# Optimization experiments

Hardware: AMD Instinct MI355X
Metric: run time of the kernel (lower is better)

Reference implementation:

```python
import jax, jax.numpy as jnp
import numpy as np

B, C, H, W = 8, 256, 64, 64
CK = C // 8  # query/key channels


def setup_inputs() -> dict:
    key = jax.random.key(0)
    ks = jax.random.split(key, 8)
    s = 1.0 / np.sqrt(C)
    return {
        "x": jax.random.normal(ks[0], (B, C, H, W), dtype=jnp.float32),
        "Wq": jax.random.normal(ks[1], (CK, C), dtype=jnp.float32) * s,
        "bq": jax.random.normal(ks[2], (CK,), dtype=jnp.float32) * 0.01,
        "Wk": jax.random.normal(ks[3], (CK, C), dtype=jnp.float32) * s,
        "bk": jax.random.normal(ks[4], (CK,), dtype=jnp.float32) * 0.01,
        "Wv": jax.random.normal(ks[5], (C, C), dtype=jnp.float32) * s,
        "bv": jax.random.normal(ks[6], (C,), dtype=jnp.float32) * 0.01,
        "gamma": jax.random.normal(ks[7], (1,), dtype=jnp.float32) * 0.1,
    }


def reference(x, Wq, bq, Wk, bk, Wv, bv, gamma):
    b, c, h, w = x.shape
    n = h * w
    xf = x.reshape(b, c, n)                       # [B,C,N]
    # 1x1 convs == channel-wise linear maps
    q = jnp.einsum('oc,bcn->bon', Wq, xf) + bq[:, None]   # [B,CK,N]
    k = jnp.einsum('oc,bcn->bon', Wk, xf) + bk[:, None]   # [B,CK,N]
    v = jnp.einsum('oc,bcn->bon', Wv, xf) + bv[:, None]   # [B,C,N]
    energy = jnp.einsum('bcm,bcn->bmn', q, k)             # [B,N,N] (query rows m)
    attn = jax.nn.softmax(energy, axis=-1)
    out = jnp.einsum('bcn,bmn->bcm', v, attn)             # value @ attn^T
    out = out.reshape(b, c, h, w)
    return gamma * out + x
```

## Files before the change

### kernel.cpp

```cpp
#include <hip/hip_runtime.h>
#include <stdint.h>

typedef unsigned short u16;
typedef unsigned int u32;
typedef __bf16 bf16_t;
typedef __bf16 bf16x4 __attribute__((ext_vector_type(4)));
typedef __bf16 bf16x8 __attribute__((ext_vector_type(8)));
typedef float f32x4 __attribute__((ext_vector_type(4)));
typedef float f32x16 __attribute__((ext_vector_type(16)));

#define LOG2E 1.4426950408889634f
#define MFMA32(a, b, c) __builtin_amdgcn_mfma_f32_32x32x16_bf16(a, b, c, 0, 0, 0)

__device__ __forceinline__ u16 f2bf(float f) {
    union { float f; unsigned int u; } v; v.f = f;
    unsigned int r = v.u + 0x7fffu + ((v.u >> 16) & 1u);
    return (u16)(r >> 16);
}

__device__ __forceinline__ bf16x8 ld8f_bf(const float* __restrict__ p) {
    float4 a = *reinterpret_cast<const float4*>(p);
    float4 b = *reinterpret_cast<const float4*>(p + 4);
    bf16x8 r;
    r[0] = (bf16_t)a.x; r[1] = (bf16_t)a.y; r[2] = (bf16_t)a.z; r[3] = (bf16_t)a.w;
    r[4] = (bf16_t)b.x; r[5] = (bf16_t)b.y; r[6] = (bf16_t)b.z; r[7] = (bf16_t)b.w;
    return r;
}

__device__ __forceinline__ u32 cvt_pk_bf16(float a, float b) {
    u32 r;
    asm("v_cvt_pk_bf16_f32 %0, %1, %2" : "=v"(r) : "v"(a), "v"(b));
    return r;
}

__device__ __forceinline__ void plane32_swap(u32& a, u32& b) {
    asm("v_permlane32_swap_b32 %0, %1" : "+v"(a), "+v"(b));
}

__device__ __forceinline__ bf16x8 pack8(const float* p) {
    u32 c0 = cvt_pk_bf16(p[0], p[1]);
    u32 c1 = cvt_pk_bf16(p[2], p[3]);
    u32 c2 = cvt_pk_bf16(p[4], p[5]);
    u32 c3 = cvt_pk_bf16(p[6], p[7]);
    plane32_swap(c0, c2);
    plane32_swap(c1, c3);
    union { u32 u[4]; bf16x8 v; } f;
    f.u[0] = c0; f.u[1] = c1; f.u[2] = c2; f.u[3] = c3;
    return f.v;
}

__device__ __forceinline__ void g2lds16(const u16* g, u16* l) {
    __builtin_amdgcn_global_load_lds(
        (const __attribute__((address_space(1))) unsigned int*)g,
        (__attribute__((address_space(3))) unsigned int*)l, 16, 0, 0);
}

__global__ __launch_bounds__(256) void k_transpose(
    const float* __restrict__ x,
    const float* __restrict__ Wq, const float* __restrict__ Wk,
    const float* __restrict__ Wv,
    u16* __restrict__ xT, u16* __restrict__ wqkb, u16* __restrict__ wvb) {
    int blk = blockIdx.x;
    int t = threadIdx.x;
    if (blk >= 2048) {
        if (blk == 2048) {
            for (int j = 0; j < 8; ++j) {
                int fg = j * 256 + t;
                int n = fg >> 5, g = fg & 31;
                const float* src = (n < 32) ? (Wq + (size_t)n * 256 + g * 8)
                                            : (Wk + (size_t)(n - 32) * 256 + g * 8);
                *reinterpret_cast<bf16x8*>(wqkb + n * 256 + ((g ^ (n & 7)) << 3)) =
                    ld8f_bf(src);
            }
        } else {
            int base = (blk - 2049) * 2048;
            for (int j = 0; j < 8; ++j) {
                int fg = base + j * 256 + t;
                int slice = fg >> 10, d = fg & 1023;
                int co = d >> 2, g2 = (d & 3) ^ (co & 3);
                *reinterpret_cast<bf16x8*>(wvb + fg * 8) =
                    ld8f_bf(Wv + (size_t)co * 256 + slice * 32 + g2 * 8);
            }
        }
        return;
    }
    __shared__ u16 tile[64][68];
    int b = blk >> 8;
    int r = blk & 255;
    int c0 = (r & 3) * 64;
    int n0 = (r >> 2) * 64;
    const float* xb = x + (size_t)b * 256 * 4096;
    u16* xTb = xT + (size_t)b * 4096 * 256;
    int lc = t >> 4;
    int l4 = (t & 15) * 4;
    #pragma unroll
    for (int p = 0; p < 4; ++p) {
        int c = lc + p * 16;
        float4 v = *reinterpret_cast<const float4*>(xb + (size_t)(c0 + c) * 4096 + n0 + l4);
        tile[c][l4 + 0] = f2bf(v.x); tile[c][l4 + 1] = f2bf(v.y);
        tile[c][l4 + 2] = f2bf(v.z); tile[c][l4 + 3] = f2bf(v.w);
    }
    __syncthreads();
    #pragma unroll
    for (int p = 0; p < 4; ++p) {
        int n = lc + p * 16;
        ushort4 v;
        v.x = tile[l4 + 0][n]; v.y = tile[l4 + 1][n];
        v.z = tile[l4 + 2][n]; v.w = tile[l4 + 3][n];
        int gslot = ((c0 + l4) >> 3) ^ ((n0 + n) & 7);
        *reinterpret_cast<ushort4*>(
            xTb + (size_t)(n0 + n) * 256 + (gslot << 3) + (l4 & 7)) = v;
    }
}

__global__ __launch_bounds__(256, 2) void k_proj(
    const u16* __restrict__ xT, const u16* __restrict__ wqkb,
    const u16* __restrict__ wvb,
    const float* __restrict__ bq, const float* __restrict__ bk,
    const float* __restrict__ bv,
    u16* __restrict__ qt, u16* __restrict__ kt, u16* __restrict__ vt) {
    __shared__ u16 Xs[64 * 256];
    __shared__ u16 Ws[64 * 256];
    __shared__ u16 Wvs[256 * 32];
    int blk = blockIdx.x;
    int b = blk & 7;
    int n0 = (blk >> 3) * 64;
    int t = threadIdx.x;
    int w = t >> 6;
    int lane = t & 63;
    int lo = lane & 15;
    int q = lane >> 4;
    const u16* xTb = xT + (size_t)b * 4096 * 256;

    #pragma unroll
    for (int p = 0; p < 8; ++p) {
        g2lds16(xTb + (size_t)n0 * 256 + (p * 256 + t) * 8, &Xs[(p * 256 + w * 64) * 8]);
        g2lds16(wqkb + (p * 256 + t) * 8, &Ws[(p * 256 + w * 64) * 8]);
    }

    f32x4 accqk[4] = {};
    f32x4 accv[16];
    #pragma unroll
    for (int i = 0; i < 16; ++i) accv[i] = f32x4{0.f, 0.f, 0.f, 0.f};

    int rowA = w * 16 + lo;
    int cw = w * 64;
    for (int c0 = 0; c0 < 256; c0 += 32) {
        __syncthreads();
        #pragma unroll
        for (int p = 0; p < 4; ++p) {
            g2lds16(wvb + (size_t)(c0 >> 5) * 8192 + (p * 256 + t) * 8,
                    &Wvs[(p * 256 + w * 64) * 8]);
        }
        __syncthreads();

        int K = c0 >> 3;
        bf16x8 a = *reinterpret_cast<const bf16x8*>(
            &Xs[(rowA * 32 + ((K + q) ^ (lo & 7))) * 8]);
        #pragma unroll
        for (int ot = 0; ot < 4; ++ot) {
            bf16x8 bb = *reinterpret_cast<const bf16x8*>(
                &Ws[((ot * 16 + lo) * 32 + ((K + q) ^ (lo & 7))) * 8]);
            accqk[ot] = __builtin_amdgcn_mfma_f32_16x16x32_bf16(a, bb, accqk[ot], 0, 0, 0);
        }
        bf16x8 xbf[4];
        #pragma unroll
        for (int nt = 0; nt < 4; ++nt)
            xbf[nt] = *reinterpret_cast<const bf16x8*>(
                &Xs[((nt * 16 + lo) * 32 + ((K + q) ^ (lo & 7))) * 8]);
        #pragma unroll
        for (int ct = 0; ct < 4; ++ct) {
            int co = cw + ct * 16 + lo;
            bf16x8 av = *reinterpret_cast<const bf16x8*>(
                &Wvs[(co * 4 + (q ^ (co & 3))) * 8]);
            #pragma unroll
            for (int nt = 0; nt < 4; ++nt)
                accv[ct * 4 + nt] = __builtin_amdgcn_mfma_f32_16x16x32_bf16(
                    av, xbf[nt], accv[ct * 4 + nt], 0, 0, 0);
        }
    }
    #pragma unroll
    for (int ot = 0; ot < 4; ++ot) {
        float bias = (ot < 2) ? bq[ot * 16 + lo] : bk[(ot - 2) * 16 + lo];
        #pragma unroll
        for (int r = 0; r < 4; ++r) {
            int n = n0 + w * 16 + q * 4 + r;
            float val = accqk[ot][r] + bias;
            if (ot < 2) qt[((size_t)b * 4096 + n) * 32 + ot * 16 + lo] = f2bf(val * LOG2E);
            else        kt[((size_t)b * 4096 + n) * 32 + (ot - 2) * 16 + lo] = f2bf(val);
        }
    }
    #pragma unroll
    for (int ct = 0; ct < 4; ++ct) {
        #pragma unroll
        for (int nt = 0; nt < 4; ++nt) {
            int nt_g = (n0 >> 4) + nt;
            #pragma unroll
            for (int r = 0; r < 4; ++r) {
                int co = cw + ct * 16 + q * 4 + r;
                float val = accv[ct * 4 + nt][r] + bv[co];
                vt[(((size_t)b * 256 + nt_g) * 256 + co) * 16 + lo] = f2bf(val);
            }
        }
    }
}

#define FLASH_PV_HALF1(FC0, FC1, Vc_)                                          \
    {                                                                          \
        bf16x8 v0_ = *reinterpret_cast<const bf16x8*>(Vc_ + gslot8);           \
        bf16x8 v1_ = *reinterpret_cast<const bf16x8*>(Vc_ + 512 + gslot8);     \
        bf16x8 v2_ = *reinterpret_cast<const bf16x8*>(Vc_ + 1024 + gslot8);    \
        bf16x8 v3_ = *reinterpret_cast<const bf16x8*>(Vc_ + 1536 + gslot8);    \
        O0 = MFMA32(v0_, FC0, O0); O1 = MFMA32(v1_, FC0, O1);                  \
        O2 = MFMA32(v2_, FC0, O2); O3 = MFMA32(v3_, FC0, O3);                  \
        bf16x8 v4_ = *reinterpret_cast<const bf16x8*>(Vc_ + 2048 + gslot8);    \
        bf16x8 v5_ = *reinterpret_cast<const bf16x8*>(Vc_ + 2560 + gslot8);    \
        bf16x8 v6_ = *reinterpret_cast<const bf16x8*>(Vc_ + 3072 + gslot8);    \
        bf16x8 v7_ = *reinterpret_cast<const bf16x8*>(Vc_ + 3584 + gslot8);    \
        O0 = MFMA32(v4_, FC1, O0); O1 = MFMA32(v5_, FC1, O1);                  \
        O2 = MFMA32(v6_, FC1, O2); O3 = MFMA32(v7_, FC1, O3);                  \
    }

#define FLASH_PV_HALF2(FC2, FC3, Vc_)                                          \
    {                                                                          \
        bf16x8 v0_ = *reinterpret_cast<const bf16x8*>(Vc_ + 4096 + gslot8);    \
        bf16x8 v1_ = *reinterpret_cast<const bf16x8*>(Vc_ + 4608 + gslot8);    \
        bf16x8 v2_ = *reinterpret_cast<const bf16x8*>(Vc_ + 5120 + gslot8);    \
        bf16x8 v3_ = *reinterpret_cast<const bf16x8*>(Vc_ + 5632 + gslot8);    \
        O0 = MFMA32(v0_, FC2, O0); O1 = MFMA32(v1_, FC2, O1);                  \
        O2 = MFMA32(v2_, FC2, O2); O3 = MFMA32(v3_, FC2, O3);                  \
        bf16x8 v4_ = *reinterpret_cast<const bf16x8*>(Vc_ + 6144 + gslot8);    \
        bf16x8 v5_ = *reinterpret_cast<const bf16x8*>(Vc_ + 6656 + gslot8);    \
        bf16x8 v6_ = *reinterpret_cast<const bf16x8*>(Vc_ + 7168 + gslot8);    \
        bf16x8 v7_ = *reinterpret_cast<const bf16x8*>(Vc_ + 7680 + gslot8);    \
        O0 = MFMA32(v4_, FC3, O0); O1 = MFMA32(v5_, FC3, O1);                  \
        O2 = MFMA32(v6_, FC3, O2); O3 = MFMA32(v7_, FC3, O3);                  \
    }

#define FLASH_ITER(S_, KC0, KC1, KC2, KC3, KN0, KN1, KN2, KN3,                 \
                   FC0, FC1, FC2, FC3, FN0, FN1, FN2, FN3, VDN)                \
    {                                                                          \
        const int s_ = (S_);                                                   \
        const u16* kp_ = kbase + (size_t)(((s_ + 2) & 63) * 2048);             \
        KN0 = *reinterpret_cast<const bf16x8*>(kp_);                           \
        KN1 = *reinterpret_cast<const bf16x8*>(kp_ + 16);                      \
        KN2 = *reinterpret_cast<const bf16x8*>(kp_ + 1024);                    \
        KN3 = *reinterpret_cast<const bf16x8*>(kp_ + 1040);                    \
        const u16* vs_ = vstage + (size_t)(s_ + 1) * 16384;                    \
        g2lds16(vs_,        VDN);                                              \
        g2lds16(vs_ + 512,  VDN + 512);                                        \
        g2lds16(vs_ + 1024, VDN + 1024);                                       \
        g2lds16(vs_ + 1536, VDN + 1536);                                       \
        f32x16 S0_ = MFMA32(KC0, qf0, z16); S0_ = MFMA32(KC1, qf1, S0_);       \
        f32x16 S1_ = MFMA32(KC2, qf0, z16); S1_ = MFMA32(KC3, qf1, S1_);       \
        const u16* Vc_ = Vs[s_ & 1];                                           \
        float p0_[16];                                                         \
        _Pragma("unroll")                                                      \
        for (int i_ = 0; i_ < 16; ++i_) {                                      \
            p0_[i_] = __builtin_amdgcn_exp2f(S0_[i_]); lsum += p0_[i_];        \
        }                                                                      \
        FN0 = pack8(p0_); FN1 = pack8(p0_ + 8);                                \
        FLASH_PV_HALF1(FC0, FC1, Vc_)                                          \
        float p1_[16];                                                         \
        _Pragma("unroll")                                                      \
        for (int i_ = 0; i_ < 16; ++i_) {                                      \
            p1_[i_] = __builtin_amdgcn_exp2f(S1_[i_]); lsum += p1_[i_];        \
        }                                                                      \
        FN2 = pack8(p1_); FN3 = pack8(p1_ + 8);                                \
        FLASH_PV_HALF2(FC2, FC3, Vc_)                                          \
        __syncthreads();                                                       \
    }

__global__ __launch_bounds__(256, 2) void k_flash(
    const u16* __restrict__ qt, const u16* __restrict__ kt,
    const u16* __restrict__ vt, const float* __restrict__ x,
    const float* __restrict__ gamma, float* __restrict__ out) {
    __shared__ u16 Vs[2][8192];
    int blk = blockIdx.x;
    int b = blk & 7;
    int rest = blk >> 3;
    int m0 = (rest & 31) * 128;
    int ch0 = (rest >> 5) * 128;
    int t = threadIdx.x;
    int w = t >> 6;
    int lane = t & 63;
    int la = lane & 31;
    int hi = lane >> 5;

    const u16* qtb = qt + (size_t)b * 4096 * 32;
    const u16* ktb = kt + (size_t)b * 4096 * 32;
    const u16* vtb = vt + (size_t)b * 256 * 256 * 16;

    int qw0 = m0 + w * 32;
    bf16x8 qf0 = *reinterpret_cast<const bf16x8*>(qtb + (size_t)(qw0 + la) * 32 + hi * 8);
    bf16x8 qf1 = *reinterpret_cast<const bf16x8*>(qtb + (size_t)(qw0 + la) * 32 + 16 + hi * 8);

    const u16* kbase = ktb + (size_t)la * 32 + hi * 8;

    int g = la * 2 + hi;
    int gslot8 = (g ^ (g >> 3)) * 8;
    int sg = lane ^ (lane >> 3);
    const u16* vstage = vtb + ((size_t)(w * 256) + ch0) * 16 + sg * 8;
    u16* vd0 = &Vs[0][w * 2048];
    u16* vd1 = &Vs[1][w * 2048];

    f32x16 O0 = {}, O1 = {}, O2 = {}, O3 = {};
    const f32x16 z16 = {};
    float lsum = 0.f;

    bf16x8 kA0, kA1, kA2, kA3, kB0, kB1, kB2, kB3;
    bf16x8 fA0, fA1, fA2, fA3, fB0, fB1, fB2, fB3;

    kA0 = *reinterpret_cast<const bf16x8*>(kbase);
    kA1 = *reinterpret_cast<const bf16x8*>(kbase + 16);
    kA2 = *reinterpret_cast<const bf16x8*>(kbase + 1024);
    kA3 = *reinterpret_cast<const bf16x8*>(kbase + 1040);
    g2lds16(vstage,        vd0);
    g2lds16(vstage + 512,  vd0 + 512);
    g2lds16(vstage + 1024, vd0 + 1024);
    g2lds16(vstage + 1536, vd0 + 1536);
    kB0 = *reinterpret_cast<const bf16x8*>(kbase + 2048);
    kB1 = *reinterpret_cast<const bf16x8*>(kbase + 2064);
    kB2 = *reinterpret_cast<const bf16x8*>(kbase + 3072);
    kB3 = *reinterpret_cast<const bf16x8*>(kbase + 3088);
    {
        f32x16 S0 = MFMA32(kA0, qf0, z16); S0 = MFMA32(kA1, qf1, S0);
        f32x16 S1 = MFMA32(kA2, qf0, z16); S1 = MFMA32(kA3, qf1, S1);
        float p0[16], p1[16];
        #pragma unroll
        for (int i = 0; i < 16; ++i) { p0[i] = __builtin_amdgcn_exp2f(S0[i]); lsum += p0[i]; }
        fA0 = pack8(p0); fA1 = pack8(p0 + 8);
        #pragma unroll
        for (int i = 0; i < 16; ++i) { p1[i] = __builtin_amdgcn_exp2f(S1[i]); lsum += p1[i]; }
        fA2 = pack8(p1); fA3 = pack8(p1 + 8);
    }
    __syncthreads();

    for (int ss = 0; ss < 31; ++ss) {
        int s0 = ss * 2;
        FLASH_ITER(s0,     kB0, kB1, kB2, kB3, kA0, kA1, kA2, kA3,
                           fA0, fA1, fA2, fA3, fB0, fB1, fB2, fB3, vd1)
        FLASH_ITER(s0 + 1, kA0, kA1, kA2, kA3, kB0, kB1, kB2, kB3,
                           fB0, fB1, fB2, fB3, fA0, fA1, fA2, fA3, vd0)
    }
    FLASH_ITER(62, kB0, kB1, kB2, kB3, kA0, kA1, kA2, kA3,
                   fA0, fA1, fA2, fA3, fB0, fB1, fB2, fB3, vd1)
    {
        const u16* Vc_ = Vs[1];
        FLASH_PV_HALF1(fB0, fB1, Vc_)
        FLASH_PV_HALF2(fB2, fB3, Vc_)
    }

    lsum += __shfl_xor(lsum, 32, 64);
    float linv = 1.0f / lsum;
    float gm = gamma[0];
    const float* xb = x + (size_t)b * 256 * 4096;
    float* ob = out + (size_t)b * 256 * 4096;
    int m = m0 + w * 32 + la;
    #pragma unroll
    for (int r = 0; r < 16; ++r) {
        int crow = (r & 3) + 8 * (r >> 2) + 4 * hi;
        size_t i0 = (size_t)(ch0 + crow) * 4096 + m;
        ob[i0]             = gm * (O0[r] * linv) + xb[i0];
        ob[i0 + 32 * 4096] = gm * (O1[r] * linv) + xb[i0 + 32 * 4096];
        ob[i0 + 64 * 4096] = gm * (O2[r] * linv) + xb[i0 + 64 * 4096];
        ob[i0 + 96 * 4096] = gm * (O3[r] * linv) + xb[i0 + 96 * 4096];
    }
}

extern "C" void kernel_launch(void* const* d_in, const int* in_sizes, int n_in,
                              void* d_out, int out_size, void* d_ws, size_t ws_size,
                              hipStream_t stream) {
    const float* x     = (const float*)d_in[0];
    const float* Wq    = (const float*)d_in[1];
    const float* bq    = (const float*)d_in[2];
    const float* Wk    = (const float*)d_in[3];
    const float* bk    = (const float*)d_in[4];
    const float* Wv    = (const float*)d_in[5];
    const float* bv    = (const float*)d_in[6];
    const float* gamma = (const float*)d_in[7];
    float* out = (float*)d_out;

    char* ws = (char*)d_ws;
    u16* xT   = (u16*)d_out;
    u16* wqkb = (u16*)d_out + 8388608;
    u16* wvb  = (u16*)d_out + 8388608 + 16384;
    u16* qt = (u16*)ws;
    u16* kt = (u16*)(ws + 2097152);
    u16* vt = (u16*)(ws + 2 * 2097152);

    k_transpose<<<2053, 256, 0, stream>>>(x, Wq, Wk, Wv, xT, wqkb, wvb);
    k_proj<<<512, 256, 0, stream>>>(xT, wqkb, wvb, bq, bk, bv, qt, kt, vt);
    k_flash<<<512, 256, 0, stream>>>(qt, kt, vt, x, gamma, out);
}
```

Measured before the change: 199.9 us.

## Halve flash channel tile to double grid; widen proj block to 128 positions

The flash kernel now gives each block 64 output channels instead of 128. That doubles the grid to 1024 blocks, halves the V staging in LDS and the output accumulators, and raises the occupancy hint to 4. The aim is better latency hiding and more waves per CU, at the cost of recomputing QK^T and the exponentials twice as often per query tile. The projection kernel switches to 512 threads covering 128 positions per block, so the Wq/Wk and Wv weight tiles are reused across more positions. s_setprio is wrapped around the PV MFMA groups to favour matrix issue.

```diff
diff --git a/kernel.cpp b/kernel.cpp
--- a/kernel.cpp
+++ b/kernel.cpp
@@ -113,18 +113,18 @@
     }
 }
 
-__global__ __launch_bounds__(256, 2) void k_proj(
+__global__ __launch_bounds__(512, 2) void k_proj(
     const u16* __restrict__ xT, const u16* __restrict__ wqkb,
     const u16* __restrict__ wvb,
     const float* __restrict__ bq, const float* __restrict__ bk,
     const float* __restrict__ bv,
     u16* __restrict__ qt, u16* __restrict__ kt, u16* __restrict__ vt) {
-    __shared__ u16 Xs[64 * 256];
+    __shared__ u16 Xs[128 * 256];
     __shared__ u16 Ws[64 * 256];
     __shared__ u16 Wvs[256 * 32];
     int blk = blockIdx.x;
     int b = blk & 7;
-    int n0 = (blk >> 3) * 64;
+    int n0 = (blk >> 3) * 128;
     int t = threadIdx.x;
     int w = t >> 6;
     int lane = t & 63;
@@ -133,10 +133,11 @@
     const u16* xTb = xT + (size_t)b * 4096 * 256;
 
     #pragma unroll
-    for (int p = 0; p < 8; ++p) {
-        g2lds16(xTb + (size_t)n0 * 256 + (p * 256 + t) * 8, &Xs[(p * 256 + w * 64) * 8]);
-        g2lds16(wqkb + (p * 256 + t) * 8, &Ws[(p * 256 + w * 64) * 8]);
-    }
+    for (int p = 0; p < 8; ++p)
+        g2lds16(xTb + (size_t)n0 * 256 + (p * 512 + t) * 8, &Xs[(p * 512 + w * 64) * 8]);
+    #pragma unroll
+    for (int p = 0; p < 4; ++p)
+        g2lds16(wqkb + (p * 512 + t) * 8, &Ws[(p * 512 + w * 64) * 8]);
 
     f32x4 accqk[4] = {};
     f32x4 accv[16];
@@ -144,14 +145,14 @@
     for (int i = 0; i < 16; ++i) accv[i] = f32x4{0.f, 0.f, 0.f, 0.f};
 
     int rowA = w * 16 + lo;
-    int cw = w * 64;
+    int cw = (w & 3) * 64;
+    int nh = (w >> 2) * 64;
     for (int c0 = 0; c0 < 256; c0 += 32) {
         __syncthreads();
         #pragma unroll
-        for (int p = 0; p < 4; ++p) {
-            g2lds16(wvb + (size_t)(c0 >> 5) * 8192 + (p * 256 + t) * 8,
-                    &Wvs[(p * 256 + w * 64) * 8]);
-        }
+        for (int p = 0; p < 2; ++p)
+            g2lds16(wvb + (size_t)(c0 >> 5) * 8192 + (p * 512 + t) * 8,
+                    &Wvs[(p * 512 + w * 64) * 8]);
         __syncthreads();
 
         int K = c0 >> 3;
@@ -167,7 +168,7 @@
         #pragma unroll
         for (int nt = 0; nt < 4; ++nt)
             xbf[nt] = *reinterpret_cast<const bf16x8*>(
-                &Xs[((nt * 16 + lo) * 32 + ((K + q) ^ (lo & 7))) * 8]);
+                &Xs[((nh + nt * 16 + lo) * 32 + ((K + q) ^ (lo & 7))) * 8]);
         #pragma unroll
         for (int ct = 0; ct < 4; ++ct) {
             int co = cw + ct * 16 + lo;
@@ -194,7 +195,7 @@
     for (int ct = 0; ct < 4; ++ct) {
         #pragma unroll
         for (int nt = 0; nt < 4; ++nt) {
-            int nt_g = (n0 >> 4) + nt;
+            int nt_g = ((n0 + nh) >> 4) + nt;
             #pragma unroll
             for (int r = 0; r < 4; ++r) {
                 int co = cw + ct * 16 + q * 4 + r;
@@ -205,36 +206,28 @@
     }
 }
 
-#define FLASH_PV_HALF1(FC0, FC1, Vc_)                                          \
+#define FLASH_PV_A(FC0, FC1, Vc_)                                              \
     {                                                                          \
         bf16x8 v0_ = *reinterpret_cast<const bf16x8*>(Vc_ + gslot8);           \
         bf16x8 v1_ = *reinterpret_cast<const bf16x8*>(Vc_ + 512 + gslot8);     \
         bf16x8 v2_ = *reinterpret_cast<const bf16x8*>(Vc_ + 1024 + gslot8);    \
         bf16x8 v3_ = *reinterpret_cast<const bf16x8*>(Vc_ + 1536 + gslot8);    \
+        __builtin_amdgcn_s_setprio(1);                                         \
         O0 = MFMA32(v0_, FC0, O0); O1 = MFMA32(v1_, FC0, O1);                  \
-        O2 = MFMA32(v2_, FC0, O2); O3 = MFMA32(v3_, FC0, O3);                  \
-        bf16x8 v4_ = *reinterpret_cast<const bf16x8*>(Vc_ + 2048 + gslot8);    \
-        bf16x8 v5_ = *reinterpret_cast<const bf16x8*>(Vc_ + 2560 + gslot8);    \
-        bf16x8 v6_ = *reinterpret_cast<const bf16x8*>(Vc_ + 3072 + gslot8);    \
-        bf16x8 v7_ = *reinterpret_cast<const bf16x8*>(Vc_ + 3584 + gslot8);    \
-        O0 = MFMA32(v4_, FC1, O0); O1 = MFMA32(v5_, FC1, O1);                  \
-        O2 = MFMA32(v6_, FC1, O2); O3 = MFMA32(v7_, FC1, O3);                  \
-    }
-
-#define FLASH_PV_HALF2(FC2, FC3, Vc_)                                          \
+        O0 = MFMA32(v2_, FC1, O0); O1 = MFMA32(v3_, FC1, O1);                  \
+        __builtin_amdgcn_s_setprio(0);                                         \
+    }
+
+#define FLASH_PV_B(FC2, FC3, Vc_)                                              \
     {                                                                          \
-        bf16x8 v0_ = *reinterpret_cast<const bf16x8*>(Vc_ + 4096 + gslot8);    \
-        bf16x8 v1_ = *reinterpret_cast<const bf16x8*>(Vc_ + 4608 + gslot8);    \
-        bf16x8 v2_ = *reinterpret_cast<const bf16x8*>(Vc_ + 5120 + gslot8);    \
-        bf16x8 v3_ = *reinterpret_cast<const bf16x8*>(Vc_ + 5632 + gslot8);    \
+        bf16x8 v0_ = *reinterpret_cast<const bf16x8*>(Vc_ + 2048 + gslot8);    \
+        bf16x8 v1_ = *reinterpret_cast<const bf16x8*>(Vc_ + 2560 + gslot8);    \
+        bf16x8 v2_ = *reinterpret_cast<const bf16x8*>(Vc_ + 3072 + gslot8);    \
+        bf16x8 v3_ = *reinterpret_cast<const bf16x8*>(Vc_ + 3584 + gslot8);    \
+        __builtin_amdgcn_s_setprio(1);                                         \
         O0 = MFMA32(v0_, FC2, O0); O1 = MFMA32(v1_, FC2, O1);                  \
-        O2 = MFMA32(v2_, FC2, O2); O3 = MFMA32(v3_, FC2, O3);                  \
-        bf16x8 v4_ = *reinterpret_cast<const bf16x8*>(Vc_ + 6144 + gslot8);    \
-        bf16x8 v5_ = *reinterpret_cast<const bf16x8*>(Vc_ + 6656 + gslot8);    \
-        bf16x8 v6_ = *reinterpret_cast<const bf16x8*>(Vc_ + 7168 + gslot8);    \
-        bf16x8 v7_ = *reinterpret_cast<const bf16x8*>(Vc_ + 7680 + gslot8);    \
-        O0 = MFMA32(v4_, FC3, O0); O1 = MFMA32(v5_, FC3, O1);                  \
-        O2 = MFMA32(v6_, FC3, O2); O3 = MFMA32(v7_, FC3, O3);                  \
+        O0 = MFMA32(v2_, FC3, O0); O1 = MFMA32(v3_, FC3, O1);                  \
+        __builtin_amdgcn_s_setprio(0);                                         \
     }
 
 #define FLASH_ITER(S_, KC0, KC1, KC2, KC3, KN0, KN1, KN2, KN3,                 \
@@ -247,10 +240,8 @@
         KN2 = *reinterpret_cast<const bf16x8*>(kp_ + 1024);                    \
         KN3 = *reinterpret_cast<const bf16x8*>(kp_ + 1040);                    \
         const u16* vs_ = vstage + (size_t)(s_ + 1) * 16384;                    \
-        g2lds16(vs_,        VDN);                                              \
-        g2lds16(vs_ + 512,  VDN + 512);                                        \
-        g2lds16(vs_ + 1024, VDN + 1024);                                       \
-        g2lds16(vs_ + 1536, VDN + 1536);                                       \
+        g2lds16(vs_,       VDN);                                               \
+        g2lds16(vs_ + 512, VDN + 512);                                         \
         f32x16 S0_ = MFMA32(KC0, qf0, z16); S0_ = MFMA32(KC1, qf1, S0_);       \
         f32x16 S1_ = MFMA32(KC2, qf0, z16); S1_ = MFMA32(KC3, qf1, S1_);       \
         const u16* Vc_ = Vs[s_ & 1];                                           \
@@ -260,27 +251,27 @@
             p0_[i_] = __builtin_amdgcn_exp2f(S0_[i_]); lsum += p0_[i_];        \
         }                                                                      \
         FN0 = pack8(p0_); FN1 = pack8(p0_ + 8);                                \
-        FLASH_PV_HALF1(FC0, FC1, Vc_)                                          \
+        FLASH_PV_A(FC0, FC1, Vc_)                                              \
         float p1_[16];                                                         \
         _Pragma("unroll")                                                      \
         for (int i_ = 0; i_ < 16; ++i_) {                                      \
             p1_[i_] = __builtin_amdgcn_exp2f(S1_[i_]); lsum += p1_[i_];        \
         }                                                                      \
         FN2 = pack8(p1_); FN3 = pack8(p1_ + 8);                                \
-        FLASH_PV_HALF2(FC2, FC3, Vc_)                                          \
+        FLASH_PV_B(FC2, FC3, Vc_)                                              \
         __syncthreads();                                                       \
     }
 
-__global__ __launch_bounds__(256, 2) void k_flash(
+__global__ __launch_bounds__(256, 4) void k_flash(
     const u16* __restrict__ qt, const u16* __restrict__ kt,
     const u16* __restrict__ vt, const float* __restrict__ x,
     const float* __restrict__ gamma, float* __restrict__ out) {
-    __shared__ u16 Vs[2][8192];
+    __shared__ u16 Vs[2][4096];
     int blk = blockIdx.x;
     int b = blk & 7;
     int rest = blk >> 3;
     int m0 = (rest & 31) * 128;
-    int ch0 = (rest >> 5) * 128;
+    int ch0 = (rest >> 5) * 64;
     int t = threadIdx.x;
     int w = t >> 6;
     int lane = t & 63;
@@ -301,10 +292,10 @@
     int gslot8 = (g ^ (g >> 3)) * 8;
     int sg = lane ^ (lane >> 3);
     const u16* vstage = vtb + ((size_t)(w * 256) + ch0) * 16 + sg * 8;
-    u16* vd0 = &Vs[0][w * 2048];
-    u16* vd1 = &Vs[1][w * 2048];
-
-    f32x16 O0 = {}, O1 = {}, O2 = {}, O3 = {};
+    u16* vd0 = &Vs[0][w * 1024];
+    u16* vd1 = &Vs[1][w * 1024];
+
+    f32x16 O0 = {}, O1 = {};
     const f32x16 z16 = {};
     float lsum = 0.f;
 
@@ -315,10 +306,8 @@
     kA1 = *reinterpret_cast<const bf16x8*>(kbase + 16);
     kA2 = *reinterpret_cast<const bf16x8*>(kbase + 1024);
     kA3 = *reinterpret_cast<const bf16x8*>(kbase + 1040);
-    g2lds16(vstage,        vd0);
-    g2lds16(vstage + 512,  vd0 + 512);
-    g2lds16(vstage + 1024, vd0 + 1024);
-    g2lds16(vstage + 1536, vd0 + 1536);
+    g2lds16(vstage,       vd0);
+    g2lds16(vstage + 512, vd0 + 512);
     kB0 = *reinterpret_cast<const bf16x8*>(kbase + 2048);
     kB1 = *reinterpret_cast<const bf16x8*>(kbase + 2064);
     kB2 = *reinterpret_cast<const bf16x8*>(kbase + 3072);
@@ -347,8 +336,8 @@
                    fA0, fA1, fA2, fA3, fB0, fB1, fB2, fB3, vd1)
     {
         const u16* Vc_ = Vs[1];
-        FLASH_PV_HALF1(fB0, fB1, Vc_)
-        FLASH_PV_HALF2(fB2, fB3, Vc_)
+        FLASH_PV_A(fB0, fB1, Vc_)
+        FLASH_PV_B(fB2, fB3, Vc_)
     }
 
     lsum += __shfl_xor(lsum, 32, 64);
@@ -363,8 +352,6 @@
         size_t i0 = (size_t)(ch0 + crow) * 4096 + m;
         ob[i0]             = gm * (O0[r] * linv) + xb[i0];
         ob[i0 + 32 * 4096] = gm * (O1[r] * linv) + xb[i0 + 32 * 4096];
-        ob[i0 + 64 * 4096] = gm * (O2[r] * linv) + xb[i0 + 64 * 4096];
-        ob[i0 + 96 * 4096] = gm * (O3[r] * linv) + xb[i0 + 96 * 4096];
     }
 }
 
@@ -390,6 +377,6 @@
     u16* vt = (u16*)(ws + 2 * 2097152);
 
     k_transpose<<<2053, 256, 0, stream>>>(x, Wq, Wk, Wv, xT, wqkb, wvb);
-    k_proj<<<512, 256, 0, stream>>>(xT, wqkb, wvb, bq, bk, bv, qt, kt, vt);
-    k_flash<<<512, 256, 0, stream>>>(qt, kt, vt, x, gamma, out);
-}
+    k_proj<<<256, 512, 0, stream>>>(xT, wqkb, wvb, bq, bk, bv, qt, kt, vt);
+    k_flash<<<1024, 256, 0, stream>>>(qt, kt, vt, x, gamma, out);
+}
```

Result: slower. 341.3 us (+70.7%).
